# Kernel optimization log

Measured on AMD Instinct MI355X. Metric: run time of the kernel, lower is better.

## Reference

```python
import jax, jax.numpy as jnp
import numpy as np


def setup_inputs() -> dict:
    key = jax.random.key(0)
    kx, ky, kA = jax.random.split(key, 3)
    B, S, L = 512, 2048, 17
    x = jax.random.normal(kx, (B, S, L), dtype=jnp.float32)
    y = jax.random.randint(ky, (B, S), 0, L, dtype=jnp.int64)
    A = (jax.random.uniform(kA, (L, L), dtype=jnp.float32) * 2.0 - 1.0) * 0.1
    return {"x": x, "y": y, "A": A}


def _viterbi(x, A):
    # x: [B,S,L] emission scores, A[k,l]: transition prev-label k -> cur-label l
    # (matches temp = dp[:, j-1, k] + A[k][l] + x[:, j, l] in the original)
    def fwd_step(prev, xt):
        # prev: [B,L] best path scores at t-1; xt: [B,L]
        scores = prev[:, :, None] + A[None, :, :]          # [B, L_prev, L_cur]
        bp = jnp.argmax(scores, axis=1)
        cur = jnp.max(scores, axis=1) + xt                 # [B,L]
        return cur, bp

    init = x[:, 0, :]
    xs = jnp.swapaxes(x[:, 1:, :], 0, 1)                   # [S-1, B, L]
    last, bps = jax.lax.scan(fwd_step, init, xs)           # bps: [S-1, B, L]

    last_lab = jnp.argmax(last, axis=1)                    # [B]

    def back_step(lab, bp):
        prev = jnp.take_along_axis(bp, lab[:, None], axis=1)[:, 0]
        return prev, prev

    # reverse scan: output at index t is the label at time t (t = 0..S-2)
    _, labs = jax.lax.scan(back_step, last_lab, bps, reverse=True)
    preds = jnp.concatenate([labs, last_lab[None, :]], axis=0)  # [S,B]
    return preds.T.astype(jnp.int32)


def _partition(x, A):
    # Faithful to MyCRF.partition_function (all-ones mask since y >= 0 everywhere):
    #   alpha0[j]    = logsumexp_k( x[0,k] + A[k,j] )
    #   alpha_t[k]   = logsumexp_l( x[t,l] + alpha_{t-1}[l] + A[l,k] ),  t = 1..S-2
    #   Z            = logsumexp_l( x[S-1,l] + alpha_{S-2}[l] )
    S = x.shape[1]
    alpha0 = jax.nn.logsumexp(x[:, 0, :, None] + A[None, :, :], axis=1)  # [B,L]

    def step(alpha, xt):
        nxt = jax.nn.logsumexp((xt + alpha)[:, :, None] + A[None, :, :], axis=1)
        return nxt, None

    xs = jnp.swapaxes(x[:, 1:S - 1, :], 0, 1)              # [S-2, B, L]
    alpha, _ = jax.lax.scan(step, alpha0, xs)
    return jax.nn.logsumexp(x[:, -1, :] + alpha, axis=1)   # [B]


def _nll(x, y, A):
    B, S, L = x.shape
    Z = _partition(x, A)
    emis = jnp.take_along_axis(x, y[:, :, None], axis=2)[:, :, 0].sum(axis=1)  # [B]
    trans = A[y[:, 1:], y[:, :-1]].sum(axis=1)             # A[cur, prev], as in loss()
    return (-(emis + trans) + Z).mean()


def reference(x, y, A):
    # training-mode forward: (most_likely_sequence, nll)
    preds = _viterbi(x, A)
    nll = _nll(x, y, A)
    return preds, nll
```

## Files before the change

kernel.cpp:

```cpp
#include <hip/hip_runtime.h>


constexpr int NL = 17;
constexpr int NS = 2048;
constexpr int NB = 512;

#define LOG2EF 1.4426950408889634f

__device__ __forceinline__ float readlane_f(float v, int l) {
  return __int_as_float(__builtin_amdgcn_readlane(__float_as_int(v), l));
}
__device__ __forceinline__ float fmax3(float a, float b, float c) {
  return fmaxf(fmaxf(a, b), c);
}

__global__ __launch_bounds__(64, 1) void crf_fwd_kernel(
    const float* __restrict__ x, const float* __restrict__ A,
    float* __restrict__ preds, double* __restrict__ wsZ) {
  __shared__ unsigned char bp[NS * NL + 128];
  __shared__ unsigned char labs[NS + 72];

  const int bid = blockIdx.x;
  const int lane = threadIdx.x;
  const int j = lane % NL;

  if (bid < NB) {
    const float* xb = x + (size_t)bid * (NS * NL);
    float a[NL];
#pragma unroll
    for (int i = 0; i < NL; ++i) a[i] = A[i * NL + j];

    const bool wr = (lane < NL);
    int bpa = wr ? (NL + lane) : (NS * NL + lane);
    const int bps4 = wr ? 4 * NL : 0;

    float cur = xb[j];
    float xr0 = xb[1 * NL + j];
    float xr1 = xb[2 * NL + j];
    float xr2 = xb[3 * NL + j];
    float xr3 = xb[4 * NL + j];

    auto vstep = [&](float& xr, int t, int off) {
      float p[NL];
#pragma unroll
      for (int i = 0; i < NL; ++i) p[i] = readlane_f(cur, i) + a[i];
      float m0 = fmax3(p[0], p[1], p[2]);
      float m1 = fmax3(p[3], p[4], p[5]);
      float m2 = fmax3(p[6], p[7], p[8]);
      float m3 = fmax3(p[9], p[10], p[11]);
      float m4 = fmax3(p[12], p[13], p[14]);
      float m5 = fmaxf(p[15], p[16]);
      float m = fmaxf(fmax3(m0, m1, m2), fmax3(m3, m4, m5));
      cur = m + xr;
      int bi = 16;
#pragma unroll
      for (int k = 15; k >= 0; --k) bi = (p[k] == m) ? k : bi;
      bp[bpa + off] = (unsigned char)bi;
      int tn = t + 4;
      tn = (tn <= NS - 1) ? tn : (NS - 1);
      xr = xb[tn * NL + j];
    };

    for (int tb = 1; tb + 3 < NS; tb += 4) {
      vstep(xr0, tb, 0);
      vstep(xr1, tb + 1, NL);
      vstep(xr2, tb + 2, 2 * NL);
      vstep(xr3, tb + 3, 3 * NL);
      bpa += bps4;
    }
    vstep(xr0, NS - 3, 0);
    vstep(xr1, NS - 2, NL);
    vstep(xr2, NS - 1, 2 * NL);

    float bv = readlane_f(cur, 0);
    int bl = 0;
#pragma unroll
    for (int i = 1; i < NL; ++i) {
      float v = readlane_f(cur, i);
      if (v > bv) { bv = v; bl = i; }
    }

    const int labsDummy = NS + lane;
    int lab = bl;
    labs[(lane == 0) ? (NS - 1) : labsDummy] = (unsigned char)lab;
    int rr0 = bp[(NS - 1) * NL + j];
    int rr1 = bp[(NS - 2) * NL + j];
    int rr2 = bp[(NS - 3) * NL + j];
    int rr3 = bp[(NS - 4) * NL + j];
    for (int tb = NS - 1; tb >= 4; tb -= 4) {
      int pt;
      lab = __builtin_amdgcn_readlane(rr0, lab);
      labs[(lane == 0) ? (tb - 1) : labsDummy] = (unsigned char)lab;
      pt = tb - 4; rr0 = bp[(pt >= 1 ? pt : 1) * NL + j];
      lab = __builtin_amdgcn_readlane(rr1, lab);
      labs[(lane == 0) ? (tb - 2) : labsDummy] = (unsigned char)lab;
      pt = tb - 5; rr1 = bp[(pt >= 1 ? pt : 1) * NL + j];
      lab = __builtin_amdgcn_readlane(rr2, lab);
      labs[(lane == 0) ? (tb - 3) : labsDummy] = (unsigned char)lab;
      pt = tb - 6; rr2 = bp[(pt >= 1 ? pt : 1) * NL + j];
      lab = __builtin_amdgcn_readlane(rr3, lab);
      labs[(lane == 0) ? (tb - 4) : labsDummy] = (unsigned char)lab;
      pt = tb - 7; rr3 = bp[(pt >= 1 ? pt : 1) * NL + j];
    }
    lab = __builtin_amdgcn_readlane(rr0, lab);
    labs[(lane == 0) ? 2 : labsDummy] = (unsigned char)lab;
    lab = __builtin_amdgcn_readlane(rr1, lab);
    labs[(lane == 0) ? 1 : labsDummy] = (unsigned char)lab;
    lab = __builtin_amdgcn_readlane(rr2, lab);
    labs[(lane == 0) ? 0 : labsDummy] = (unsigned char)lab;

    float* pb = preds + (size_t)bid * NS;
    for (int k = lane; k < NS; k += 64) pb[k] = (float)labs[k];
  } else {
    const int b = bid - NB;
    const float* xb = x + (size_t)b * (NS * NL);

    float E[NL];
#pragma unroll
    for (int i = 0; i < NL; ++i)
      E[i] = __builtin_amdgcn_exp2f(A[i * NL + j] * LOG2EF);

    float g = __builtin_amdgcn_exp2f(xb[j] * LOG2EF);
    double base = 0.0;
    float xr0 = xb[1 * NL + j] * LOG2EF;
    float xr1 = xb[2 * NL + j] * LOG2EF;
    float xr2 = xb[3 * NL + j] * LOG2EF;
    float xr3 = xb[4 * NL + j] * LOG2EF;

    auto pstep = [&](float& xr, int t) {
      float gg[NL];
#pragma unroll
      for (int i = 0; i < NL; ++i) gg[i] = readlane_f(g, i);
      float s0 = gg[0] * E[0];
      float s1 = gg[1] * E[1];
      float s2 = gg[2] * E[2];
      float s3 = gg[3] * E[3];
#pragma unroll
      for (int i = 4; i + 3 < NL; i += 4) {
        s0 = fmaf(gg[i + 0], E[i + 0], s0);
        s1 = fmaf(gg[i + 1], E[i + 1], s1);
        s2 = fmaf(gg[i + 2], E[i + 2], s2);
        s3 = fmaf(gg[i + 3], E[i + 3], s3);
      }
      s0 = fmaf(gg[16], E[16], s0);
      float s = (s0 + s1) + (s2 + s3);
      float w = __builtin_amdgcn_logf(s) + xr;
      float w0 = readlane_f(w, 0);
      base += (double)w0;
      g = __builtin_amdgcn_exp2f(w - w0);
      int tn = t + 4;
      tn = (tn <= NS - 1) ? tn : (NS - 1);
      xr = xb[tn * NL + j] * LOG2EF;
    };

    for (int tb = 1; tb + 3 < NS; tb += 4) {
      pstep(xr0, tb);
      pstep(xr1, tb + 1);
      pstep(xr2, tb + 2);
      pstep(xr3, tb + 3);
    }
    pstep(xr0, NS - 3);
    pstep(xr1, NS - 2);
    pstep(xr2, NS - 1);

    float sg = readlane_f(g, 0);
#pragma unroll
    for (int i = 1; i < NL; ++i) sg += readlane_f(g, i);
    if (lane == 0)
      wsZ[b] = (base + (double)__builtin_amdgcn_logf(sg)) *
               0.6931471805599453;
  }
}

__global__ __launch_bounds__(64, 1) void crf_gather_kernel(
    const float* __restrict__ x, const int* __restrict__ y,
    const float* __restrict__ A, float* __restrict__ wsS) {
  const int bq = blockIdx.x;
  const int b = bq >> 2;
  const int q = bq & 3;
  const int lane = threadIdx.x;
  const float* xb = x + (size_t)b * (NS * NL);
  const int* yb = y + (size_t)b * NS;
  const int t0 = q * 512;
  float sum = 0.f;
#pragma unroll
  for (int it = 0; it < 8; ++it) {
    int t = t0 + it * 64 + lane;
    int yt = yb[t];
    sum += xb[t * NL + yt];
    if (t >= 1) sum += A[yt * NL + yb[t - 1]];
  }
#pragma unroll
  for (int off = 32; off >= 1; off >>= 1) sum += __shfl_xor(sum, off);
  if (lane == 0) wsS[bq] = sum;
}

__global__ __launch_bounds__(512, 1) void crf_final_kernel(
    const double* __restrict__ wsZ, const float* __restrict__ wsS,
    float* __restrict__ outNll) {
  __shared__ double sm[NB];
  const int b = threadIdx.x;
  float s = (wsS[4 * b] + wsS[4 * b + 1]) + (wsS[4 * b + 2] + wsS[4 * b + 3]);
  sm[b] = wsZ[b] - (double)s;
  __syncthreads();
  for (int off = NB / 2; off >= 1; off >>= 1) {
    if (b < off) sm[b] += sm[b + off];
    __syncthreads();
  }
  if (b == 0) outNll[0] = (float)(sm[0] * (1.0 / NB));
}

extern "C" void kernel_launch(void* const* d_in, const int* in_sizes, int n_in,
                              void* d_out, int out_size, void* d_ws,
                              size_t ws_size, hipStream_t stream) {
  const float* x = (const float*)d_in[0];
  const int* y = (const int*)d_in[1];
  const float* A = (const float*)d_in[2];
  float* out = (float*)d_out;
  double* wsZ = (double*)d_ws;
  float* wsS = (float*)((char*)d_ws + NB * sizeof(double));

  crf_fwd_kernel<<<dim3(2 * NB), dim3(64), 0, stream>>>(x, A, out, wsZ);
  crf_gather_kernel<<<dim3(4 * NB), dim3(64), 0, stream>>>(x, y, A, wsS);
  crf_final_kernel<<<dim3(1), dim3(512), 0, stream>>>(wsZ, wsS,
                                                      out + (size_t)NB * NS);
}
```

Before: 514.7 us.

## Drop forward argmax by storing scores to global and recomputing backpointers in backtrace

The Viterbi forward pass no longer computes a 17-way argmax per step. Each step writes the running scores and the per-label max to a global workspace, and the backtrace rebuilds each backpointer with a ballot over equality tests against the stored max. The gold-path gather is folded into the partition blocks, which removes the separate gather kernel and one launch. In exchange it adds about 150 MB of global writes and reads of workspace, and it falls back to the old kernels when the workspace is too small.

```diff
diff --git a/kernel.cpp b/kernel.cpp
--- a/kernel.cpp
+++ b/kernel.cpp
@@ -4,6 +4,7 @@
 constexpr int NL = 17;
 constexpr int NS = 2048;
 constexpr int NB = 512;
+constexpr int ZROW = 36;
 
 #define LOG2EF 1.4426950408889634f
 
@@ -14,33 +15,39 @@
   return fmaxf(fmaxf(a, b), c);
 }
 
-__global__ __launch_bounds__(64, 1) void crf_fwd_kernel(
-    const float* __restrict__ x, const float* __restrict__ A,
-    float* __restrict__ preds, double* __restrict__ wsZ) {
-  __shared__ unsigned char bp[NS * NL + 128];
+__global__ __launch_bounds__(64, 1) void crf_fused_kernel(
+    const float* __restrict__ x, const int* __restrict__ y,
+    const float* __restrict__ A, float* __restrict__ preds,
+    float* __restrict__ zm, double* __restrict__ wsP) {
   __shared__ unsigned char labs[NS + 72];
-
   const int bid = blockIdx.x;
   const int lane = threadIdx.x;
   const int j = lane % NL;
 
   if (bid < NB) {
     const float* xb = x + (size_t)bid * (NS * NL);
+    float* zmb = zm + (size_t)bid * ((size_t)NS * ZROW);
     float a[NL];
 #pragma unroll
     for (int i = 0; i < NL; ++i) a[i] = A[i * NL + j];
-
-    const bool wr = (lane < NL);
-    int bpa = wr ? (NL + lane) : (NS * NL + lane);
-    const int bps4 = wr ? 4 * NL : 0;
+    const bool lt17 = (lane < 17);
+    const int zslot = (lane < 34) ? lane : 34;
 
     float cur = xb[j];
-    float xr0 = xb[1 * NL + j];
-    float xr1 = xb[2 * NL + j];
-    float xr2 = xb[3 * NL + j];
-    float xr3 = xb[4 * NL + j];
-
-    auto vstep = [&](float& xr, int t, int off) {
+    zmb[zslot] = cur;
+    float* zp = zmb + ZROW + zslot;
+    const float* xpf = xb + 9 * NL + j;
+
+    float xq0 = xb[1 * NL + j];
+    float xq1 = xb[2 * NL + j];
+    float xq2 = xb[3 * NL + j];
+    float xq3 = xb[4 * NL + j];
+    float xq4 = xb[5 * NL + j];
+    float xq5 = xb[6 * NL + j];
+    float xq6 = xb[7 * NL + j];
+    float xq7 = xb[8 * NL + j];
+
+    auto vstep = [&](float& xr) {
       float p[NL];
 #pragma unroll
       for (int i = 0; i < NL; ++i) p[i] = readlane_f(cur, i) + a[i];
@@ -52,25 +59,37 @@
       float m5 = fmaxf(p[15], p[16]);
       float m = fmaxf(fmax3(m0, m1, m2), fmax3(m3, m4, m5));
       cur = m + xr;
-      int bi = 16;
-#pragma unroll
-      for (int k = 15; k >= 0; --k) bi = (p[k] == m) ? k : bi;
-      bp[bpa + off] = (unsigned char)bi;
-      int tn = t + 4;
-      tn = (tn <= NS - 1) ? tn : (NS - 1);
+      *zp = lt17 ? cur : m;
+      zp += ZROW;
+      xr = *xpf;
+      xpf += NL;
+    };
+    for (int g = 0; g < 254; ++g) {
+      vstep(xq0); vstep(xq1); vstep(xq2); vstep(xq3);
+      vstep(xq4); vstep(xq5); vstep(xq6); vstep(xq7);
+    }
+    auto vstep_t = [&](float& xr, int t) {
+      float p[NL];
+#pragma unroll
+      for (int i = 0; i < NL; ++i) p[i] = readlane_f(cur, i) + a[i];
+      float m0 = fmax3(p[0], p[1], p[2]);
+      float m1 = fmax3(p[3], p[4], p[5]);
+      float m2 = fmax3(p[6], p[7], p[8]);
+      float m3 = fmax3(p[9], p[10], p[11]);
+      float m4 = fmax3(p[12], p[13], p[14]);
+      float m5 = fmaxf(p[15], p[16]);
+      float m = fmaxf(fmax3(m0, m1, m2), fmax3(m3, m4, m5));
+      cur = m + xr;
+      *zp = lt17 ? cur : m;
+      zp += ZROW;
+      int tn = (t + 8 <= NS - 1) ? (t + 8) : (NS - 1);
       xr = xb[tn * NL + j];
     };
-
-    for (int tb = 1; tb + 3 < NS; tb += 4) {
-      vstep(xr0, tb, 0);
-      vstep(xr1, tb + 1, NL);
-      vstep(xr2, tb + 2, 2 * NL);
-      vstep(xr3, tb + 3, 3 * NL);
-      bpa += bps4;
-    }
-    vstep(xr0, NS - 3, 0);
-    vstep(xr1, NS - 2, NL);
-    vstep(xr2, NS - 1, 2 * NL);
+    vstep_t(xq0, 2033); vstep_t(xq1, 2034); vstep_t(xq2, 2035);
+    vstep_t(xq3, 2036); vstep_t(xq4, 2037); vstep_t(xq5, 2038);
+    vstep_t(xq6, 2039); vstep_t(xq7, 2040); vstep_t(xq0, 2041);
+    vstep_t(xq1, 2042); vstep_t(xq2, 2043); vstep_t(xq3, 2044);
+    vstep_t(xq4, 2045); vstep_t(xq5, 2046); vstep_t(xq6, 2047);
 
     float bv = readlane_f(cur, 0);
     int bl = 0;
@@ -79,42 +98,71 @@
       float v = readlane_f(cur, i);
       if (v > bv) { bv = v; bl = i; }
     }
-
-    const int labsDummy = NS + lane;
+    labs[(lane == 0) ? (NS - 1) : (NS + lane)] = (unsigned char)bl;
+
+    asm volatile("s_waitcnt vmcnt(0)" ::: "memory");
+    float aT[NL];
+#pragma unroll
+    for (int c = 0; c < NL; ++c) aT[c] = A[j * NL + c];
+    float r0 = zmb[(size_t)2040 * ZROW + zslot];
+    float r1 = zmb[(size_t)2041 * ZROW + zslot];
+    float r2 = zmb[(size_t)2042 * ZROW + zslot];
+    float r3 = zmb[(size_t)2043 * ZROW + zslot];
+    float r4 = zmb[(size_t)2044 * ZROW + zslot];
+    float r5 = zmb[(size_t)2045 * ZROW + zslot];
+    float r6 = zmb[(size_t)2046 * ZROW + zslot];
+    float r7 = zmb[(size_t)2047 * ZROW + zslot];
+    const float* rp = zmb + (size_t)2039 * ZROW + zslot;
     int lab = bl;
-    labs[(lane == 0) ? (NS - 1) : labsDummy] = (unsigned char)lab;
-    int rr0 = bp[(NS - 1) * NL + j];
-    int rr1 = bp[(NS - 2) * NL + j];
-    int rr2 = bp[(NS - 3) * NL + j];
-    int rr3 = bp[(NS - 4) * NL + j];
-    for (int tb = NS - 1; tb >= 4; tb -= 4) {
-      int pt;
-      lab = __builtin_amdgcn_readlane(rr0, lab);
-      labs[(lane == 0) ? (tb - 1) : labsDummy] = (unsigned char)lab;
-      pt = tb - 4; rr0 = bp[(pt >= 1 ? pt : 1) * NL + j];
-      lab = __builtin_amdgcn_readlane(rr1, lab);
-      labs[(lane == 0) ? (tb - 2) : labsDummy] = (unsigned char)lab;
-      pt = tb - 5; rr1 = bp[(pt >= 1 ? pt : 1) * NL + j];
-      lab = __builtin_amdgcn_readlane(rr2, lab);
-      labs[(lane == 0) ? (tb - 3) : labsDummy] = (unsigned char)lab;
-      pt = tb - 6; rr2 = bp[(pt >= 1 ? pt : 1) * NL + j];
-      lab = __builtin_amdgcn_readlane(rr3, lab);
-      labs[(lane == 0) ? (tb - 4) : labsDummy] = (unsigned char)lab;
-      pt = tb - 7; rr3 = bp[(pt >= 1 ? pt : 1) * NL + j];
-    }
-    lab = __builtin_amdgcn_readlane(rr0, lab);
-    labs[(lane == 0) ? 2 : labsDummy] = (unsigned char)lab;
-    lab = __builtin_amdgcn_readlane(rr1, lab);
-    labs[(lane == 0) ? 1 : labsDummy] = (unsigned char)lab;
-    lab = __builtin_amdgcn_readlane(rr2, lab);
-    labs[(lane == 0) ? 0 : labsDummy] = (unsigned char)lab;
+
+    auto bt_iter = [&](float& rM, float rZ, int t, bool pf) {
+      float tgt = readlane_f(rM, 17 + lab);
+      float s0 = (lab & 1) ? aT[1] : aT[0];
+      float s1 = (lab & 1) ? aT[3] : aT[2];
+      float s2 = (lab & 1) ? aT[5] : aT[4];
+      float s3 = (lab & 1) ? aT[7] : aT[6];
+      float s4 = (lab & 1) ? aT[9] : aT[8];
+      float s5 = (lab & 1) ? aT[11] : aT[10];
+      float s6 = (lab & 1) ? aT[13] : aT[12];
+      float s7 = (lab & 1) ? aT[15] : aT[14];
+      float u0 = (lab & 2) ? s1 : s0;
+      float u1 = (lab & 2) ? s3 : s2;
+      float u2 = (lab & 2) ? s5 : s4;
+      float u3 = (lab & 2) ? s7 : s6;
+      float v0 = (lab & 4) ? u1 : u0;
+      float v1 = (lab & 4) ? u3 : u2;
+      float w0 = (lab & 8) ? v1 : v0;
+      float asel = (lab & 16) ? aT[16] : w0;
+      float pv = rZ + asel;
+      unsigned long long mm = __ballot(pv == tgt) & 0x1FFFFull;
+      lab = __ffsll(mm) - 1;
+      labs[(lane == 0) ? (t - 1) : (NS + lane)] = (unsigned char)lab;
+      if (pf) { rM = *rp; rp -= ZROW; }
+    };
+    int t0 = 2047;
+    for (int g = 0; g < 255; ++g, t0 -= 8) {
+      bt_iter(r7, r6, t0 - 0, true);
+      bt_iter(r6, r5, t0 - 1, true);
+      bt_iter(r5, r4, t0 - 2, true);
+      bt_iter(r4, r3, t0 - 3, true);
+      bt_iter(r3, r2, t0 - 4, true);
+      bt_iter(r2, r1, t0 - 5, true);
+      bt_iter(r1, r0, t0 - 6, true);
+      bt_iter(r0, r7, t0 - 7, true);
+    }
+    bt_iter(r7, r6, 7, false);
+    bt_iter(r6, r5, 6, false);
+    bt_iter(r5, r4, 5, false);
+    bt_iter(r4, r3, 4, false);
+    bt_iter(r3, r2, 3, false);
+    bt_iter(r2, r1, 2, false);
+    bt_iter(r1, r0, 1, false);
 
     float* pb = preds + (size_t)bid * NS;
     for (int k = lane; k < NS; k += 64) pb[k] = (float)labs[k];
   } else {
     const int b = bid - NB;
     const float* xb = x + (size_t)b * (NS * NL);
-
     float E[NL];
 #pragma unroll
     for (int i = 0; i < NL; ++i)
@@ -152,32 +200,174 @@
       tn = (tn <= NS - 1) ? tn : (NS - 1);
       xr = xb[tn * NL + j] * LOG2EF;
     };
-
     for (int tb = 1; tb + 3 < NS; tb += 4) {
-      pstep(xr0, tb);
-      pstep(xr1, tb + 1);
-      pstep(xr2, tb + 2);
-      pstep(xr3, tb + 3);
-    }
-    pstep(xr0, NS - 3);
-    pstep(xr1, NS - 2);
-    pstep(xr2, NS - 1);
-
+      pstep(xr0, tb); pstep(xr1, tb + 1); pstep(xr2, tb + 2); pstep(xr3, tb + 3);
+    }
+    pstep(xr0, NS - 3); pstep(xr1, NS - 2); pstep(xr2, NS - 1);
+
+    float sg = readlane_f(g, 0);
+#pragma unroll
+    for (int i = 1; i < NL; ++i) sg += readlane_f(g, i);
+    double Zd = (base + (double)__builtin_amdgcn_logf(sg)) * 0.6931471805599453;
+
+    const int* yb = y + (size_t)b * NS;
+    float gsum = 0.f;
+    for (int it = 0; it < 32; ++it) {
+      int t = it * 64 + lane;
+      int yt = yb[t];
+      int tp = (t >= 1) ? (t - 1) : 0;
+      int yp = yb[tp];
+      float e = xb[t * NL + yt];
+      float tr = (t >= 1) ? A[yt * NL + yp] : 0.0f;
+      gsum += e + tr;
+    }
+#pragma unroll
+    for (int off = 32; off >= 1; off >>= 1) gsum += __shfl_xor(gsum, off);
+    if (lane == 0) wsP[b] = Zd - (double)gsum;
+  }
+}
+
+__global__ __launch_bounds__(512, 1) void crf_mean_kernel(
+    const double* __restrict__ wsP, float* __restrict__ outNll) {
+  __shared__ double sm[NB];
+  const int i = threadIdx.x;
+  sm[i] = wsP[i];
+  __syncthreads();
+  for (int off = NB / 2; off >= 1; off >>= 1) {
+    if (i < off) sm[i] += sm[i + off];
+    __syncthreads();
+  }
+  if (i == 0) outNll[0] = (float)(sm[0] * (1.0 / NB));
+}
+
+__global__ __launch_bounds__(64, 1) void crf_fwd_fb(
+    const float* __restrict__ x, const float* __restrict__ A,
+    float* __restrict__ preds, double* __restrict__ wsZ) {
+  __shared__ unsigned char bp[NS * NL + 128];
+  __shared__ unsigned char labs[NS + 72];
+  const int bid = blockIdx.x;
+  const int lane = threadIdx.x;
+  const int j = lane % NL;
+  if (bid < NB) {
+    const float* xb = x + (size_t)bid * (NS * NL);
+    float a[NL];
+#pragma unroll
+    for (int i = 0; i < NL; ++i) a[i] = A[i * NL + j];
+    const bool wr = (lane < NL);
+    int bpa = wr ? (NL + lane) : (NS * NL + lane);
+    const int bps4 = wr ? 4 * NL : 0;
+    float cur = xb[j];
+    float xr0 = xb[1 * NL + j], xr1 = xb[2 * NL + j];
+    float xr2 = xb[3 * NL + j], xr3 = xb[4 * NL + j];
+    auto vstep = [&](float& xr, int t, int off) {
+      float p[NL];
+#pragma unroll
+      for (int i = 0; i < NL; ++i) p[i] = readlane_f(cur, i) + a[i];
+      float m0 = fmax3(p[0], p[1], p[2]), m1 = fmax3(p[3], p[4], p[5]);
+      float m2 = fmax3(p[6], p[7], p[8]), m3 = fmax3(p[9], p[10], p[11]);
+      float m4 = fmax3(p[12], p[13], p[14]), m5 = fmaxf(p[15], p[16]);
+      float m = fmaxf(fmax3(m0, m1, m2), fmax3(m3, m4, m5));
+      cur = m + xr;
+      int bi = 16;
+#pragma unroll
+      for (int k = 15; k >= 0; --k) bi = (p[k] == m) ? k : bi;
+      bp[bpa + off] = (unsigned char)bi;
+      int tn = t + 4;
+      tn = (tn <= NS - 1) ? tn : (NS - 1);
+      xr = xb[tn * NL + j];
+    };
+    for (int tb = 1; tb + 3 < NS; tb += 4) {
+      vstep(xr0, tb, 0); vstep(xr1, tb + 1, NL);
+      vstep(xr2, tb + 2, 2 * NL); vstep(xr3, tb + 3, 3 * NL);
+      bpa += bps4;
+    }
+    vstep(xr0, NS - 3, 0); vstep(xr1, NS - 2, NL); vstep(xr2, NS - 1, 2 * NL);
+    float bv = readlane_f(cur, 0);
+    int bl = 0;
+#pragma unroll
+    for (int i = 1; i < NL; ++i) {
+      float v = readlane_f(cur, i);
+      if (v > bv) { bv = v; bl = i; }
+    }
+    const int labsDummy = NS + lane;
+    int lab = bl;
+    labs[(lane == 0) ? (NS - 1) : labsDummy] = (unsigned char)lab;
+    int rr0 = bp[(NS - 1) * NL + j], rr1 = bp[(NS - 2) * NL + j];
+    int rr2 = bp[(NS - 3) * NL + j], rr3 = bp[(NS - 4) * NL + j];
+    for (int tb = NS - 1; tb >= 4; tb -= 4) {
+      int pt;
+      lab = __builtin_amdgcn_readlane(rr0, lab);
+      labs[(lane == 0) ? (tb - 1) : labsDummy] = (unsigned char)lab;
+      pt = tb - 4; rr0 = bp[(pt >= 1 ? pt : 1) * NL + j];
+      lab = __builtin_amdgcn_readlane(rr1, lab);
+      labs[(lane == 0) ? (tb - 2) : labsDummy] = (unsigned char)lab;
+      pt = tb - 5; rr1 = bp[(pt >= 1 ? pt : 1) * NL + j];
+      lab = __builtin_amdgcn_readlane(rr2, lab);
+      labs[(lane == 0) ? (tb - 3) : labsDummy] = (unsigned char)lab;
+      pt = tb - 6; rr2 = bp[(pt >= 1 ? pt : 1) * NL + j];
+      lab = __builtin_amdgcn_readlane(rr3, lab);
+      labs[(lane == 0) ? (tb - 4) : labsDummy] = (unsigned char)lab;
+      pt = tb - 7; rr3 = bp[(pt >= 1 ? pt : 1) * NL + j];
+    }
+    lab = __builtin_amdgcn_readlane(rr0, lab);
+    labs[(lane == 0) ? 2 : labsDummy] = (unsigned char)lab;
+    lab = __builtin_amdgcn_readlane(rr1, lab);
+    labs[(lane == 0) ? 1 : labsDummy] = (unsigned char)lab;
+    lab = __builtin_amdgcn_readlane(rr2, lab);
+    labs[(lane == 0) ? 0 : labsDummy] = (unsigned char)lab;
+    float* pb = preds + (size_t)bid * NS;
+    for (int k = lane; k < NS; k += 64) pb[k] = (float)labs[k];
+  } else {
+    const int b = bid - NB;
+    const float* xb = x + (size_t)b * (NS * NL);
+    float E[NL];
+#pragma unroll
+    for (int i = 0; i < NL; ++i)
+      E[i] = __builtin_amdgcn_exp2f(A[i * NL + j] * LOG2EF);
+    float g = __builtin_amdgcn_exp2f(xb[j] * LOG2EF);
+    double base = 0.0;
+    float xr0 = xb[1 * NL + j] * LOG2EF, xr1 = xb[2 * NL + j] * LOG2EF;
+    float xr2 = xb[3 * NL + j] * LOG2EF, xr3 = xb[4 * NL + j] * LOG2EF;
+    auto pstep = [&](float& xr, int t) {
+      float gg[NL];
+#pragma unroll
+      for (int i = 0; i < NL; ++i) gg[i] = readlane_f(g, i);
+      float s0 = gg[0] * E[0], s1 = gg[1] * E[1];
+      float s2 = gg[2] * E[2], s3 = gg[3] * E[3];
+#pragma unroll
+      for (int i = 4; i + 3 < NL; i += 4) {
+        s0 = fmaf(gg[i + 0], E[i + 0], s0);
+        s1 = fmaf(gg[i + 1], E[i + 1], s1);
+        s2 = fmaf(gg[i + 2], E[i + 2], s2);
+        s3 = fmaf(gg[i + 3], E[i + 3], s3);
+      }
+      s0 = fmaf(gg[16], E[16], s0);
+      float s = (s0 + s1) + (s2 + s3);
+      float w = __builtin_amdgcn_logf(s) + xr;
+      float w0 = readlane_f(w, 0);
+      base += (double)w0;
+      g = __builtin_amdgcn_exp2f(w - w0);
+      int tn = t + 4;
+      tn = (tn <= NS - 1) ? tn : (NS - 1);
+      xr = xb[tn * NL + j] * LOG2EF;
+    };
+    for (int tb = 1; tb + 3 < NS; tb += 4) {
+      pstep(xr0, tb); pstep(xr1, tb + 1); pstep(xr2, tb + 2); pstep(xr3, tb + 3);
+    }
+    pstep(xr0, NS - 3); pstep(xr1, NS - 2); pstep(xr2, NS - 1);
     float sg = readlane_f(g, 0);
 #pragma unroll
     for (int i = 1; i < NL; ++i) sg += readlane_f(g, i);
     if (lane == 0)
-      wsZ[b] = (base + (double)__builtin_amdgcn_logf(sg)) *
-               0.6931471805599453;
-  }
-}
-
-__global__ __launch_bounds__(64, 1) void crf_gather_kernel(
+      wsZ[b] = (base + (double)__builtin_amdgcn_logf(sg)) * 0.6931471805599453;
+  }
+}
+
+__global__ __launch_bounds__(64, 1) void crf_gather_fb(
     const float* __restrict__ x, const int* __restrict__ y,
     const float* __restrict__ A, float* __restrict__ wsS) {
   const int bq = blockIdx.x;
-  const int b = bq >> 2;
-  const int q = bq & 3;
+  const int b = bq >> 2, q = bq & 3;
   const int lane = threadIdx.x;
   const float* xb = x + (size_t)b * (NS * NL);
   const int* yb = y + (size_t)b * NS;
@@ -195,7 +385,7 @@
   if (lane == 0) wsS[bq] = sum;
 }
 
-__global__ __launch_bounds__(512, 1) void crf_final_kernel(
+__global__ __launch_bounds__(512, 1) void crf_final_fb(
     const double* __restrict__ wsZ, const float* __restrict__ wsS,
     float* __restrict__ outNll) {
   __shared__ double sm[NB];
@@ -217,11 +407,21 @@
   const int* y = (const int*)d_in[1];
   const float* A = (const float*)d_in[2];
   float* out = (float*)d_out;
-  double* wsZ = (double*)d_ws;
-  float* wsS = (float*)((char*)d_ws + NB * sizeof(double));
-
-  crf_fwd_kernel<<<dim3(2 * NB), dim3(64), 0, stream>>>(x, A, out, wsZ);
-  crf_gather_kernel<<<dim3(4 * NB), dim3(64), 0, stream>>>(x, y, A, wsS);
-  crf_final_kernel<<<dim3(1), dim3(512), 0, stream>>>(wsZ, wsS,
-                                                      out + (size_t)NB * NS);
-}
+
+  const size_t need = 4096 + (size_t)NB * NS * ZROW * sizeof(float);
+  if (ws_size >= need) {
+    double* wsP = (double*)d_ws;
+    float* zm = (float*)((char*)d_ws + 4096);
+    crf_fused_kernel<<<dim3(2 * NB), dim3(64), 0, stream>>>(x, y, A, out, zm,
+                                                            wsP);
+    crf_mean_kernel<<<dim3(1), dim3(512), 0, stream>>>(wsP,
+                                                       out + (size_t)NB * NS);
+  } else {
+    double* wsZ = (double*)d_ws;
+    float* wsS = (float*)((char*)d_ws + NB * sizeof(double));
+    crf_fwd_fb<<<dim3(2 * NB), dim3(64), 0, stream>>>(x, A, out, wsZ);
+    crf_gather_fb<<<dim3(4 * NB), dim3(64), 0, stream>>>(x, y, A, wsS);
+    crf_final_fb<<<dim3(1), dim3(512), 0, stream>>>(wsZ, wsS,
+                                                    out + (size_t)NB * NS);
+  }
+}
```

Measured after the change: 604.7 us. +17.5%, slower.

## Move Viterbi argmax off serial chain into parallel backpointer pass via stored scores

Applied to the files above, without the earlier changes.

The forward Viterbi recurrence no longer computes backpointer argmax per step. It only computes max scores and writes them to a global workspace. A new 512-thread kernel recomputes the argmax for all timesteps in parallel across 8 waves from the stored scores, then does the backtrace. The gather/emission sum is folded into the partition blocks, removing one kernel launch. This shortens the latency-bound serial chain at the cost of roughly 75 MB of extra global write and read traffic and an additional kernel.

```diff
diff --git a/kernel.cpp b/kernel.cpp
--- a/kernel.cpp
+++ b/kernel.cpp
@@ -4,6 +4,7 @@
 constexpr int NL = 17;
 constexpr int NS = 2048;
 constexpr int NB = 512;
+constexpr int ZR = 18;
 
 #define LOG2EF 1.4426950408889634f
 
@@ -14,33 +15,37 @@
   return fmaxf(fmaxf(a, b), c);
 }
 
-__global__ __launch_bounds__(64, 1) void crf_fwd_kernel(
-    const float* __restrict__ x, const float* __restrict__ A,
-    float* __restrict__ preds, double* __restrict__ wsZ) {
-  __shared__ unsigned char bp[NS * NL + 128];
-  __shared__ unsigned char labs[NS + 72];
-
+__global__ __launch_bounds__(64, 1) void crf_fwd2_kernel(
+    const float* __restrict__ x, const int* __restrict__ y,
+    const float* __restrict__ A, float* __restrict__ zws,
+    double* __restrict__ wsP) {
   const int bid = blockIdx.x;
   const int lane = threadIdx.x;
   const int j = lane % NL;
 
   if (bid < NB) {
     const float* xb = x + (size_t)bid * (NS * NL);
+    float* zb = zws + (size_t)bid * ((size_t)NS * ZR);
     float a[NL];
 #pragma unroll
     for (int i = 0; i < NL; ++i) a[i] = A[i * NL + j];
-
-    const bool wr = (lane < NL);
-    int bpa = wr ? (NL + lane) : (NS * NL + lane);
-    const int bps4 = wr ? 4 * NL : 0;
+    const int zslot = (lane < 17) ? lane : 17;
 
     float cur = xb[j];
-    float xr0 = xb[1 * NL + j];
-    float xr1 = xb[2 * NL + j];
-    float xr2 = xb[3 * NL + j];
-    float xr3 = xb[4 * NL + j];
-
-    auto vstep = [&](float& xr, int t, int off) {
+    zb[zslot] = cur;
+    float* zp = zb + ZR + zslot;
+    const float* xpf = xb + 9 * NL + j;
+
+    float xq0 = xb[1 * NL + j];
+    float xq1 = xb[2 * NL + j];
+    float xq2 = xb[3 * NL + j];
+    float xq3 = xb[4 * NL + j];
+    float xq4 = xb[5 * NL + j];
+    float xq5 = xb[6 * NL + j];
+    float xq6 = xb[7 * NL + j];
+    float xq7 = xb[8 * NL + j];
+
+    auto vstep = [&](float& xr) {
       float p[NL];
 #pragma unroll
       for (int i = 0; i < NL; ++i) p[i] = readlane_f(cur, i) + a[i];
@@ -52,34 +57,169 @@
       float m5 = fmaxf(p[15], p[16]);
       float m = fmaxf(fmax3(m0, m1, m2), fmax3(m3, m4, m5));
       cur = m + xr;
-      int bi = 16;
-#pragma unroll
-      for (int k = 15; k >= 0; --k) bi = (p[k] == m) ? k : bi;
-      bp[bpa + off] = (unsigned char)bi;
+      *zp = cur;
+      zp += ZR;
+      xr = *xpf;
+      xpf += NL;
+    };
+    for (int g = 0; g < 254; ++g) {
+      vstep(xq0); vstep(xq1); vstep(xq2); vstep(xq3);
+      vstep(xq4); vstep(xq5); vstep(xq6); vstep(xq7);
+    }
+    auto vstep_t = [&](float& xr, int t) {
+      float p[NL];
+#pragma unroll
+      for (int i = 0; i < NL; ++i) p[i] = readlane_f(cur, i) + a[i];
+      float m0 = fmax3(p[0], p[1], p[2]);
+      float m1 = fmax3(p[3], p[4], p[5]);
+      float m2 = fmax3(p[6], p[7], p[8]);
+      float m3 = fmax3(p[9], p[10], p[11]);
+      float m4 = fmax3(p[12], p[13], p[14]);
+      float m5 = fmaxf(p[15], p[16]);
+      float m = fmaxf(fmax3(m0, m1, m2), fmax3(m3, m4, m5));
+      cur = m + xr;
+      *zp = cur;
+      zp += ZR;
+      int tn = (t + 8 <= NS - 1) ? (t + 8) : (NS - 1);
+      xr = xb[tn * NL + j];
+    };
+    vstep_t(xq0, 2033); vstep_t(xq1, 2034); vstep_t(xq2, 2035);
+    vstep_t(xq3, 2036); vstep_t(xq4, 2037); vstep_t(xq5, 2038);
+    vstep_t(xq6, 2039); vstep_t(xq7, 2040); vstep_t(xq0, 2041);
+    vstep_t(xq1, 2042); vstep_t(xq2, 2043); vstep_t(xq3, 2044);
+    vstep_t(xq4, 2045); vstep_t(xq5, 2046); vstep_t(xq6, 2047);
+  } else {
+    const int b = bid - NB;
+    const float* xb = x + (size_t)b * (NS * NL);
+    float E[NL];
+#pragma unroll
+    for (int i = 0; i < NL; ++i)
+      E[i] = __builtin_amdgcn_exp2f(A[i * NL + j] * LOG2EF);
+
+    float g = __builtin_amdgcn_exp2f(xb[j] * LOG2EF);
+    double base = 0.0;
+    float xr0 = xb[1 * NL + j] * LOG2EF;
+    float xr1 = xb[2 * NL + j] * LOG2EF;
+    float xr2 = xb[3 * NL + j] * LOG2EF;
+    float xr3 = xb[4 * NL + j] * LOG2EF;
+
+    auto pstep = [&](float& xr, int t) {
+      float gg[NL];
+#pragma unroll
+      for (int i = 0; i < NL; ++i) gg[i] = readlane_f(g, i);
+      float s0 = gg[0] * E[0];
+      float s1 = gg[1] * E[1];
+      float s2 = gg[2] * E[2];
+      float s3 = gg[3] * E[3];
+#pragma unroll
+      for (int i = 4; i + 3 < NL; i += 4) {
+        s0 = fmaf(gg[i + 0], E[i + 0], s0);
+        s1 = fmaf(gg[i + 1], E[i + 1], s1);
+        s2 = fmaf(gg[i + 2], E[i + 2], s2);
+        s3 = fmaf(gg[i + 3], E[i + 3], s3);
+      }
+      s0 = fmaf(gg[16], E[16], s0);
+      float s = (s0 + s1) + (s2 + s3);
+      float w = __builtin_amdgcn_logf(s) + xr;
+      float w0 = readlane_f(w, 0);
+      base += (double)w0;
+      g = __builtin_amdgcn_exp2f(w - w0);
       int tn = t + 4;
       tn = (tn <= NS - 1) ? tn : (NS - 1);
-      xr = xb[tn * NL + j];
+      xr = xb[tn * NL + j] * LOG2EF;
     };
-
     for (int tb = 1; tb + 3 < NS; tb += 4) {
-      vstep(xr0, tb, 0);
-      vstep(xr1, tb + 1, NL);
-      vstep(xr2, tb + 2, 2 * NL);
-      vstep(xr3, tb + 3, 3 * NL);
-      bpa += bps4;
-    }
-    vstep(xr0, NS - 3, 0);
-    vstep(xr1, NS - 2, NL);
-    vstep(xr2, NS - 1, 2 * NL);
-
-    float bv = readlane_f(cur, 0);
+      pstep(xr0, tb); pstep(xr1, tb + 1); pstep(xr2, tb + 2); pstep(xr3, tb + 3);
+    }
+    pstep(xr0, NS - 3); pstep(xr1, NS - 2); pstep(xr2, NS - 1);
+
+    float sg = readlane_f(g, 0);
+#pragma unroll
+    for (int i = 1; i < NL; ++i) sg += readlane_f(g, i);
+    double Zd = (base + (double)__builtin_amdgcn_logf(sg)) * 0.6931471805599453;
+
+    const int* yb = y + (size_t)b * NS;
+    float gsum = 0.f;
+    for (int it = 0; it < 32; ++it) {
+      int t = it * 64 + lane;
+      int yt = yb[t];
+      int tp = (t >= 1) ? (t - 1) : 0;
+      int yp = yb[tp];
+      float e = xb[t * NL + yt];
+      float tr = (t >= 1) ? A[yt * NL + yp] : 0.0f;
+      gsum += e + tr;
+    }
+#pragma unroll
+    for (int off = 32; off >= 1; off >>= 1) gsum += __shfl_xor(gsum, off);
+    if (lane == 0) wsP[b] = Zd - (double)gsum;
+  }
+}
+
+__global__ __launch_bounds__(512, 1) void crf_bt2_kernel(
+    const float* __restrict__ zws, const float* __restrict__ A,
+    float* __restrict__ preds) {
+  __shared__ unsigned char bp[NS * NL + 64];
+  __shared__ unsigned char labs[NS + 72];
+  const int b = blockIdx.x;
+  const int tid = threadIdx.x;
+  const int lane = tid & 63;
+  const int w = tid >> 6;
+  const int j = lane % NL;
+  const float* zb = zws + (size_t)b * ((size_t)NS * ZR);
+
+  float a[NL];
+#pragma unroll
+  for (int i = 0; i < NL; ++i) a[i] = A[i * NL + j];
+  const int zl = (lane < 18) ? lane : 17;
+  const bool jok = (lane < 17);
+  const int dummyB = NS * NL + lane;
+
+  int t = 1 + w;
+  float zr0 = zb[(size_t)(w + 0) * ZR + zl];
+  float zr1 = zb[(size_t)(w + 8) * ZR + zl];
+  float zr2 = zb[(size_t)(w + 16) * ZR + zl];
+  float zr3 = zb[(size_t)(w + 24) * ZR + zl];
+  float zr4 = zb[(size_t)(w + 32) * ZR + zl];
+  float zr5 = zb[(size_t)(w + 40) * ZR + zl];
+  float zr6 = zb[(size_t)(w + 48) * ZR + zl];
+  float zr7 = zb[(size_t)(w + 56) * ZR + zl];
+
+  auto row = [&](float& zr) {
+    int trow = (t <= NS - 1) ? t : (NS - 1);
+    float p[NL];
+#pragma unroll
+    for (int i = 0; i < NL; ++i) p[i] = readlane_f(zr, i) + a[i];
+    float m0 = fmax3(p[0], p[1], p[2]);
+    float m1 = fmax3(p[3], p[4], p[5]);
+    float m2 = fmax3(p[6], p[7], p[8]);
+    float m3 = fmax3(p[9], p[10], p[11]);
+    float m4 = fmax3(p[12], p[13], p[14]);
+    float m5 = fmaxf(p[15], p[16]);
+    float m = fmaxf(fmax3(m0, m1, m2), fmax3(m3, m4, m5));
+    int bi = 16;
+#pragma unroll
+    for (int k = 15; k >= 0; --k) bi = (p[k] == m) ? k : bi;
+    bp[jok ? (trow * NL + j) : dummyB] = (unsigned char)bi;
+    int nz = t - 1 + 64;
+    nz = (nz <= NS - 1) ? nz : (NS - 1);
+    zr = zb[(size_t)nz * ZR + zl];
+    t += 8;
+  };
+  for (int g = 0; g < 32; ++g) {
+    row(zr0); row(zr1); row(zr2); row(zr3);
+    row(zr4); row(zr5); row(zr6); row(zr7);
+  }
+  __syncthreads();
+
+  if (tid < 64) {
+    float zf = zb[(size_t)(NS - 1) * ZR + zl];
+    float bv = readlane_f(zf, 0);
     int bl = 0;
 #pragma unroll
     for (int i = 1; i < NL; ++i) {
-      float v = readlane_f(cur, i);
+      float v = readlane_f(zf, i);
       if (v > bv) { bv = v; bl = i; }
     }
-
     const int labsDummy = NS + lane;
     int lab = bl;
     labs[(lane == 0) ? (NS - 1) : labsDummy] = (unsigned char)lab;
@@ -108,106 +248,24 @@
     labs[(lane == 0) ? 1 : labsDummy] = (unsigned char)lab;
     lab = __builtin_amdgcn_readlane(rr2, lab);
     labs[(lane == 0) ? 0 : labsDummy] = (unsigned char)lab;
-
-    float* pb = preds + (size_t)bid * NS;
-    for (int k = lane; k < NS; k += 64) pb[k] = (float)labs[k];
-  } else {
-    const int b = bid - NB;
-    const float* xb = x + (size_t)b * (NS * NL);
-
-    float E[NL];
-#pragma unroll
-    for (int i = 0; i < NL; ++i)
-      E[i] = __builtin_amdgcn_exp2f(A[i * NL + j] * LOG2EF);
-
-    float g = __builtin_amdgcn_exp2f(xb[j] * LOG2EF);
-    double base = 0.0;
-    float xr0 = xb[1 * NL + j] * LOG2EF;
-    float xr1 = xb[2 * NL + j] * LOG2EF;
-    float xr2 = xb[3 * NL + j] * LOG2EF;
-    float xr3 = xb[4 * NL + j] * LOG2EF;
-
-    auto pstep = [&](float& xr, int t) {
-      float gg[NL];
-#pragma unroll
-      for (int i = 0; i < NL; ++i) gg[i] = readlane_f(g, i);
-      float s0 = gg[0] * E[0];
-      float s1 = gg[1] * E[1];
-      float s2 = gg[2] * E[2];
-      float s3 = gg[3] * E[3];
-#pragma unroll
-      for (int i = 4; i + 3 < NL; i += 4) {
-        s0 = fmaf(gg[i + 0], E[i + 0], s0);
-        s1 = fmaf(gg[i + 1], E[i + 1], s1);
-        s2 = fmaf(gg[i + 2], E[i + 2], s2);
-        s3 = fmaf(gg[i + 3], E[i + 3], s3);
-      }
-      s0 = fmaf(gg[16], E[16], s0);
-      float s = (s0 + s1) + (s2 + s3);
-      float w = __builtin_amdgcn_logf(s) + xr;
-      float w0 = readlane_f(w, 0);
-      base += (double)w0;
-      g = __builtin_amdgcn_exp2f(w - w0);
-      int tn = t + 4;
-      tn = (tn <= NS - 1) ? tn : (NS - 1);
-      xr = xb[tn * NL + j] * LOG2EF;
-    };
-
-    for (int tb = 1; tb + 3 < NS; tb += 4) {
-      pstep(xr0, tb);
-      pstep(xr1, tb + 1);
-      pstep(xr2, tb + 2);
-      pstep(xr3, tb + 3);
-    }
-    pstep(xr0, NS - 3);
-    pstep(xr1, NS - 2);
-    pstep(xr2, NS - 1);
-
-    float sg = readlane_f(g, 0);
-#pragma unroll
-    for (int i = 1; i < NL; ++i) sg += readlane_f(g, i);
-    if (lane == 0)
-      wsZ[b] = (base + (double)__builtin_amdgcn_logf(sg)) *
-               0.6931471805599453;
-  }
-}
-
-__global__ __launch_bounds__(64, 1) void crf_gather_kernel(
-    const float* __restrict__ x, const int* __restrict__ y,
-    const float* __restrict__ A, float* __restrict__ wsS) {
-  const int bq = blockIdx.x;
-  const int b = bq >> 2;
-  const int q = bq & 3;
-  const int lane = threadIdx.x;
-  const float* xb = x + (size_t)b * (NS * NL);
-  const int* yb = y + (size_t)b * NS;
-  const int t0 = q * 512;
-  float sum = 0.f;
-#pragma unroll
-  for (int it = 0; it < 8; ++it) {
-    int t = t0 + it * 64 + lane;
-    int yt = yb[t];
-    sum += xb[t * NL + yt];
-    if (t >= 1) sum += A[yt * NL + yb[t - 1]];
-  }
-#pragma unroll
-  for (int off = 32; off >= 1; off >>= 1) sum += __shfl_xor(sum, off);
-  if (lane == 0) wsS[bq] = sum;
-}
-
-__global__ __launch_bounds__(512, 1) void crf_final_kernel(
-    const double* __restrict__ wsZ, const float* __restrict__ wsS,
-    float* __restrict__ outNll) {
+  }
+  __syncthreads();
+
+  float* pb = preds + (size_t)b * NS;
+  for (int k = tid; k < NS; k += 512) pb[k] = (float)labs[k];
+}
+
+__global__ __launch_bounds__(512, 1) void crf_mean_kernel(
+    const double* __restrict__ wsP, float* __restrict__ outNll) {
   __shared__ double sm[NB];
-  const int b = threadIdx.x;
-  float s = (wsS[4 * b] + wsS[4 * b + 1]) + (wsS[4 * b + 2] + wsS[4 * b + 3]);
-  sm[b] = wsZ[b] - (double)s;
+  const int i = threadIdx.x;
+  sm[i] = wsP[i];
   __syncthreads();
   for (int off = NB / 2; off >= 1; off >>= 1) {
-    if (b < off) sm[b] += sm[b + off];
+    if (i < off) sm[i] += sm[i + off];
     __syncthreads();
   }
-  if (b == 0) outNll[0] = (float)(sm[0] * (1.0 / NB));
+  if (i == 0) outNll[0] = (float)(sm[0] * (1.0 / NB));
 }
 
 extern "C" void kernel_launch(void* const* d_in, const int* in_sizes, int n_in,
@@ -217,11 +275,11 @@
   const int* y = (const int*)d_in[1];
   const float* A = (const float*)d_in[2];
   float* out = (float*)d_out;
-  double* wsZ = (double*)d_ws;
-  float* wsS = (float*)((char*)d_ws + NB * sizeof(double));
-
-  crf_fwd_kernel<<<dim3(2 * NB), dim3(64), 0, stream>>>(x, A, out, wsZ);
-  crf_gather_kernel<<<dim3(4 * NB), dim3(64), 0, stream>>>(x, y, A, wsS);
-  crf_final_kernel<<<dim3(1), dim3(512), 0, stream>>>(wsZ, wsS,
-                                                      out + (size_t)NB * NS);
-}
+  double* wsP = (double*)d_ws;
+  float* zws = (float*)((char*)d_ws + 4096);
+
+  crf_fwd2_kernel<<<dim3(2 * NB), dim3(64), 0, stream>>>(x, y, A, zws, wsP);
+  crf_bt2_kernel<<<dim3(NB), dim3(512), 0, stream>>>(zws, A, out);
+  crf_mean_kernel<<<dim3(1), dim3(512), 0, stream>>>(wsP,
+                                                     out + (size_t)NB * NS);
+}
```

New measurement: 569.5 us. +10.6%, slower.
